# Optimization experiments

Measured on AMD Instinct MI355X. Metric: run time of the kernel, lower is better.

The kernel has to match this reference:

```python
import jax, jax.numpy as jnp
import numpy as np

PILLAR_WH = np.array([0.16, 0.16], np.float32)
MAX_POINTS = 100
MAX_PILLARS = 12000
MIN_XYZ = np.array([-51.2, -51.2, -5.0], np.float32)
MAX_XYZ = np.array([51.2, 51.2, 3.0], np.float32)
PAD_VALUE = 0.0
NGRID = np.ceil((MAX_XYZ[:2] - MIN_XYZ[:2]) / PILLAR_WH).astype(np.int32)  # [640, 640]
WH_N = (2.0 * PILLAR_WH / (MAX_XYZ[:2] - MIN_XYZ[:2])).astype(np.float32)  # pillar size in normalized coords
MIN_XY_N = (MIN_XYZ[:2] / MAX_XYZ[:2]).astype(np.float32)  # = [-1, -1]


def setup_inputs() -> dict:
    key = jax.random.key(0)
    B, P = 4, 50000
    k1, k2, k3 = jax.random.split(key, 3)
    # x,y restricted to [-8, 8] m so occupied pillars (<=100x100=10000) <= max_pillars,
    # making the torch module's random pillar subsampling a deterministic no-op.
    xy = jax.random.uniform(k1, (B, P, 2), minval=-8.0, maxval=8.0, dtype=jnp.float32)
    z = jax.random.uniform(k2, (B, P, 1), minval=-5.0, maxval=3.0, dtype=jnp.float32)
    r = jax.random.uniform(k3, (B, P, 1), dtype=jnp.float32)
    return {"point_clouds": jnp.concatenate([xy, z, r], axis=-1)}


def _per_sample(pc, pidx):
    # pc: (P, 4) normalized points; pidx: (P,) int32 pillar ids
    P = pc.shape[0]
    u, inv = jnp.unique(pidx, size=MAX_PILLARS, fill_value=-1, return_inverse=True)
    counts = jax.ops.segment_sum(jnp.ones((P,), jnp.int32), inv, num_segments=MAX_PILLARS)
    sums = jax.ops.segment_sum(pc[:, :3], inv, num_segments=MAX_PILLARS)
    mean = sums / jnp.maximum(counts, 1).astype(pc.dtype)[:, None]
    # stable sort points by pillar id; rank = position within pillar
    order = jnp.argsort(inv)
    seg = inv[order]
    pts = pc[order]
    start = jnp.cumsum(counts) - counts  # exclusive prefix of counts
    rank = jnp.arange(P, dtype=jnp.int32) - start[seg]
    in_cap = rank < MAX_POINTS
    flat = jnp.where(in_cap, seg * MAX_POINTS + rank, MAX_PILLARS * MAX_POINTS)  # OOB -> dropped
    buf = jnp.zeros((MAX_PILLARS * MAX_POINTS, 4), pc.dtype).at[flat].set(pts, mode='drop')
    occ = jnp.zeros((MAX_PILLARS * MAX_POINTS,), bool).at[flat].set(True, mode='drop')
    buf = buf.reshape(MAX_PILLARS, MAX_POINTS, 4)
    occ = occ.reshape(MAX_PILLARS, MAX_POINTS)
    ij = jnp.stack([u % NGRID[0], u // NGRID[0]], axis=-1).astype(pc.dtype)
    centers = jnp.asarray(MIN_XY_N) + ij * jnp.asarray(WH_N) + jnp.asarray(WH_N) * 0.5
    feat_c = jnp.abs(buf[..., :3] - mean[:, None, :])  # |xyz - pillar mean|
    feat_p = centers[:, None, :] - buf[..., :2]        # pillar center offset
    out = jnp.concatenate([buf, feat_c, feat_p], axis=-1)  # (max_pillars, max_points, 9)
    out = jnp.where(occ[..., None], out, jnp.asarray(PAD_VALUE, pc.dtype))
    return out, u


def reference(point_clouds):
    pc = point_clouds
    xyz_n = 2.0 * (pc[..., :3] - jnp.asarray(MIN_XYZ)) / jnp.asarray(MAX_XYZ - MIN_XYZ) - 1.0
    pc_n = jnp.concatenate([xyz_n, pc[..., 3:]], axis=-1)
    ij = jnp.minimum(
        jnp.floor((xyz_n[..., :2] - jnp.asarray(MIN_XY_N)) / jnp.asarray(WH_N)),
        jnp.asarray(NGRID, xyz_n.dtype) - 1.0,
    ).astype(jnp.int32)
    pidx = ij[..., 1] * int(NGRID[0]) + ij[..., 0]
    out, pillars = jax.vmap(_per_sample)(pc_n, pidx)
    return out, pillars
```

## Files before the change

kernel.cpp:

```cpp
#include <hip/hip_runtime.h>

#define NB 4
#define GRID_X 640
#define NCELL (GRID_X*GRID_X)
#define NWORD (NCELL/32)
#define MAXPIL 12000
#define MAXPTS 100
#define SCAN_BLK 256
#define NBLKA (NWORD/SCAN_BLK)

typedef unsigned short u16;
typedef unsigned int   u32;

__device__ __forceinline__ float bf16rt(float f) {
    u32 u = __builtin_bit_cast(u32, f);
    u32 r = ((u + 0x7FFFu + ((u >> 16) & 1u)) >> 16) << 16;
    return __builtin_bit_cast(float, r);
}

__device__ __forceinline__ float opaquef(float x) { asm volatile("" : "+v"(x)); return x; }

#define R102 0.009765625f
#define RWH  320.000030517578125f
__device__ __host__ constexpr float WH_N_C() { return (2.0f*0.16f)/(51.2f-(-51.2f)); }

__device__ __forceinline__ float norm_x(float v) {
    float p = 2.0f*(v + 51.2f) * R102;
    return opaquef(p) - 1.0f;
}
__device__ __forceinline__ float norm_z(float v) {
    float p = 2.0f*(v + 5.0f) * 0.125f;
    return opaquef(p) - 1.0f;
}

__device__ __forceinline__ int cell_of(float xn, float yn) {
    float fx = fminf(fmaxf(floorf((xn + 1.0f) * RWH), 0.0f), 639.0f);
    float fy = fminf(fmaxf(floorf((yn + 1.0f) * RWH), 0.0f), 639.0f);
    return (int)fy * GRID_X + (int)fx;
}

__global__ void k_init(int4* __restrict__ zero4, int nz4,
                       float* __restrict__ pillars_f, int* __restrict__ slotCell, int npil) {
    int i = blockIdx.x*blockDim.x + threadIdx.x;
    if (i < nz4) zero4[i] = make_int4(0,0,0,0);
    if (i < npil) { pillars_f[i] = -1.0f; slotCell[i] = -1; }
}

__global__ void k_mask(const float4* __restrict__ pc, int P, u32* __restrict__ occMask) {
    int i = blockIdx.x*blockDim.x + threadIdx.x;
    if (i >= NB*P) return;
    float4 pt = pc[i];
    int cell = cell_of(norm_x(pt.x), norm_x(pt.y));
    int b = i / P;
    atomicOr(&occMask[b*NWORD + (cell >> 5)], 1u << (cell & 31));
}

__global__ void k_scanA(const u32* __restrict__ occMask, int* __restrict__ scanBlk) {
    __shared__ int lds[SCAN_BLK];
    int blk = blockIdx.x % NBLKA;
    int b   = blockIdx.x / NBLKA;
    int w   = blk*SCAN_BLK + threadIdx.x;
    lds[threadIdx.x] = __popc(occMask[b*NWORD + w]);
    __syncthreads();
    for (int d = SCAN_BLK/2; d > 0; d >>= 1) {
        if (threadIdx.x < d) lds[threadIdx.x] += lds[threadIdx.x + d];
        __syncthreads();
    }
    if (threadIdx.x == 0) scanBlk[b*NBLKA + blk] = lds[0];
}

__global__ void k_scanB(int* __restrict__ scanBlk) {
    int b = blockIdx.x;
    if (threadIdx.x == 0) {
        int acc = 0;
        for (int i = 0; i < NBLKA; i++) {
            int v = scanBlk[b*NBLKA + i];
            scanBlk[b*NBLKA + i] = acc;
            acc += v;
        }
    }
}

__global__ void k_scanC(const u32* __restrict__ occMask, const int* __restrict__ scanBlk,
                        int* __restrict__ wordPrefix, float* __restrict__ pillars_f,
                        int* __restrict__ slotCell) {
    __shared__ int lds[SCAN_BLK];
    int blk = blockIdx.x % NBLKA;
    int b   = blockIdx.x / NBLKA;
    int tid = threadIdx.x;
    int w   = blk*SCAN_BLK + tid;
    u32 m = occMask[b*NWORD + w];
    int pop = __popc(m);
    lds[tid] = pop;
    __syncthreads();
    for (int d = 1; d < SCAN_BLK; d <<= 1) {
        int t = (tid >= d) ? lds[tid - d] : 0;
        __syncthreads();
        lds[tid] += t;
        __syncthreads();
    }
    int prefix = scanBlk[b*NBLKA + blk] + lds[tid] - pop;
    wordPrefix[b*NWORD + w] = prefix;
    int wbase = w << 5;
    int slot = prefix;
    while (m) {
        int bit = __ffs(m) - 1;
        m &= m - 1;
        if (slot < MAXPIL) {
            int cell = wbase + bit;
            slotCell[b*MAXPIL + slot] = cell;
            pillars_f[b*MAXPIL + slot] = bf16rt((float)cell);
        }
        slot++;
    }
}

__global__ void k_scatter(const float4* __restrict__ pc, int P,
                          const u32* __restrict__ occMask, const int* __restrict__ wordPrefix,
                          int* __restrict__ slotCnt, u16* __restrict__ idx16) {
    int i = blockIdx.x*blockDim.x + threadIdx.x;
    if (i >= NB*P) return;
    int b = i / P;
    int p = i - b*P;
    float4 pt = pc[i];
    int cell = cell_of(norm_x(pt.x), norm_x(pt.y));
    int w = cell >> 5, bit = cell & 31;
    u32 m = occMask[b*NWORD + w];
    int slot = wordPrefix[b*NWORD + w] + __popc(m & ((1u << bit) - 1u));
    if (slot >= MAXPIL) return;
    int g = b*MAXPIL + slot;
    int pos = atomicAdd(&slotCnt[g], 1);
    if (pos < MAXPTS) idx16[(size_t)g*MAXPTS + pos] = (u16)p;
}

__global__ __launch_bounds__(64) void k_write(const float4* __restrict__ pc, int P,
                        const int* __restrict__ slotCell, const int* __restrict__ slotCnt,
                        const u16* __restrict__ idx16, float* __restrict__ out) {
    __shared__ __align__(16) float tile[MAXPTS*9];
    __shared__ int sIdx[MAXPTS];
    __shared__ float sx[MAXPTS], sy[MAXPTS], sz[MAXPTS], sr[MAXPTS];
    int g = blockIdx.x;
    int b = g / MAXPIL;
    int lane = threadIdx.x;
    float4* out4 = (float4*)out + (size_t)g*225;
    int u = slotCell[g];
    if (u < 0) {
        float4 z = make_float4(0.f,0.f,0.f,0.f);
        for (int i = lane; i < 225; i += 64) out4[i] = z;
        return;
    }
    int ntot = slotCnt[g];
    int n = min(ntot, MAXPTS);

    float4* t4 = (float4*)tile;
    for (int i = lane; i < 225; i += 64) t4[i] = make_float4(0.f,0.f,0.f,0.f);

    float ax = 0.f, ay = 0.f, az = 0.f;
    for (int j = lane; j < n; j += 64) {
        int p = idx16[(size_t)g*MAXPTS + j];
        sIdx[j] = p;
        float4 pt = pc[b*P + p];
        float xn = norm_x(pt.x);
        float yn = norm_x(pt.y);
        float zn = norm_z(pt.z);
        sx[j] = xn; sy[j] = yn; sz[j] = zn; sr[j] = pt.w;
        ax += xn; ay += yn; az += zn;
    }
    for (int msk = 1; msk < 64; msk <<= 1) {
        ax += __shfl_xor(ax, msk);
        ay += __shfl_xor(ay, msk);
        az += __shfl_xor(az, msk);
    }
    float den = (float)max(ntot, 1);
    float mx = ax/den, my = ay/den, mz = az/den;
    const float wh = WH_N_C();
    float cx = -1.0f + (float)(u % GRID_X)*wh + wh*0.5f;
    float cy = -1.0f + (float)(u / GRID_X)*wh + wh*0.5f;
    __syncthreads();

    for (int j = lane; j < n; j += 64) {
        int p = sIdx[j];
        int rk = 0;
        for (int k = 0; k < n; k++) rk += (sIdx[k] < p) ? 1 : 0;
        float xn = sx[j], yn = sy[j], zn = sz[j];
        float* e = &tile[rk*9];
        e[0] = xn; e[1] = yn; e[2] = zn; e[3] = sr[j];
        e[4] = fabsf(xn - mx); e[5] = fabsf(yn - my); e[6] = fabsf(zn - mz);
        e[7] = cx - xn; e[8] = cy - yn;
    }
    __syncthreads();
    for (int i = lane; i < 225; i += 64) out4[i] = t4[i];
}

extern "C" void kernel_launch(void* const* d_in, const int* in_sizes, int n_in,
                              void* d_out, int out_size, void* d_ws, size_t ws_size,
                              hipStream_t stream) {
    const float4* pc = (const float4*)d_in[0];
    int P = in_sizes[0] / (NB*4);
    float* out = (float*)d_out;
    float* pillars_f = out + (size_t)NB*MAXPIL*MAXPTS*9;

    u32* occMask   = (u32*)d_ws;
    int* slotCnt   = (int*)(occMask + NB*NWORD);
    int* wordPrefix= slotCnt + NB*MAXPIL;
    int* scanBlk   = wordPrefix + NB*NWORD;
    int* slotCell  = scanBlk + 256;
    u16* idx16     = (u16*)(slotCell + NB*MAXPIL);

    int nzero = NB*NWORD + NB*MAXPIL;
    int nz4 = nzero / 4;
    int initThreads = nz4 > NB*MAXPIL ? nz4 : NB*MAXPIL;

    k_init<<<(initThreads+255)/256, 256, 0, stream>>>((int4*)occMask, nz4, pillars_f, slotCell, NB*MAXPIL);
    k_mask<<<(NB*P+255)/256, 256, 0, stream>>>(pc, P, occMask);
    k_scanA<<<NB*NBLKA, SCAN_BLK, 0, stream>>>(occMask, scanBlk);
    k_scanB<<<NB, 64, 0, stream>>>(scanBlk);
    k_scanC<<<NB*NBLKA, SCAN_BLK, 0, stream>>>(occMask, scanBlk, wordPrefix, pillars_f, slotCell);
    k_scatter<<<(NB*P+255)/256, 256, 0, stream>>>(pc, P, occMask, wordPrefix, slotCnt, idx16);
    k_write<<<NB*MAXPIL, 64, 0, stream>>>(pc, P, slotCell, slotCnt, idx16, out);
}
```

Baseline: 226.9 us.

## Merge three-pass scan into one block-per-sample kernel and cache point cell ids

Replaces the three scan kernels (block reduce, serial block prefix, block scan) with a single 512-thread kernel per sample. Each thread scans 25 mask words in registers, and the same kernel also zeroes slot counts and fills the unused pillar slots. k_mask now stores each point's cell id, so k_scatter reads it back instead of reloading the point and recomputing the cell. This removes two launches and the serial scanB pass, but runs the scan on only 4 blocks and adds 800 KB of cell-id writes and reads.

```diff
diff --git a/kernel.cpp b/kernel.cpp
--- a/kernel.cpp
+++ b/kernel.cpp
@@ -6,8 +6,8 @@
 #define NWORD (NCELL/32)
 #define MAXPIL 12000
 #define MAXPTS 100
-#define SCAN_BLK 256
-#define NBLKA (NWORD/SCAN_BLK)
+#define SCAN_T 512
+#define WPT (NWORD/SCAN_T)
 
 typedef unsigned short u16;
 typedef unsigned int   u32;
@@ -39,91 +39,78 @@
     return (int)fy * GRID_X + (int)fx;
 }
 
-__global__ void k_init(int4* __restrict__ zero4, int nz4,
-                       float* __restrict__ pillars_f, int* __restrict__ slotCell, int npil) {
+__global__ void k_init(int4* __restrict__ zero4, int nz4) {
     int i = blockIdx.x*blockDim.x + threadIdx.x;
     if (i < nz4) zero4[i] = make_int4(0,0,0,0);
-    if (i < npil) { pillars_f[i] = -1.0f; slotCell[i] = -1; }
-}
-
-__global__ void k_mask(const float4* __restrict__ pc, int P, u32* __restrict__ occMask) {
+}
+
+__global__ void k_mask(const float4* __restrict__ pc, int P, u32* __restrict__ occMask,
+                       int* __restrict__ cellId) {
     int i = blockIdx.x*blockDim.x + threadIdx.x;
     if (i >= NB*P) return;
     float4 pt = pc[i];
     int cell = cell_of(norm_x(pt.x), norm_x(pt.y));
+    cellId[i] = cell;
     int b = i / P;
     atomicOr(&occMask[b*NWORD + (cell >> 5)], 1u << (cell & 31));
 }
 
-__global__ void k_scanA(const u32* __restrict__ occMask, int* __restrict__ scanBlk) {
-    __shared__ int lds[SCAN_BLK];
-    int blk = blockIdx.x % NBLKA;
-    int b   = blockIdx.x / NBLKA;
-    int w   = blk*SCAN_BLK + threadIdx.x;
-    lds[threadIdx.x] = __popc(occMask[b*NWORD + w]);
+__global__ __launch_bounds__(SCAN_T) void k_scan(const u32* __restrict__ occMask,
+        int* __restrict__ wordPrefix, int* __restrict__ slotCnt,
+        int* __restrict__ slotCell, float* __restrict__ pillars_f) {
+    __shared__ int lds[SCAN_T];
+    int b = blockIdx.x;
+    int t = threadIdx.x;
+    const u32* mask = occMask + b*NWORD;
+    int base = t*WPT;
+    u32 w[WPT];
+#pragma unroll
+    for (int i = 0; i < WPT; i++) w[i] = mask[base + i];
+    for (int i = t; i < MAXPIL; i += SCAN_T) slotCnt[b*MAXPIL + i] = 0;
+    int sum = 0;
+#pragma unroll
+    for (int i = 0; i < WPT; i++) sum += __popc(w[i]);
+    lds[t] = sum;
     __syncthreads();
-    for (int d = SCAN_BLK/2; d > 0; d >>= 1) {
-        if (threadIdx.x < d) lds[threadIdx.x] += lds[threadIdx.x + d];
+    for (int d = 1; d < SCAN_T; d <<= 1) {
+        int v = (t >= d) ? lds[t - d] : 0;
         __syncthreads();
-    }
-    if (threadIdx.x == 0) scanBlk[b*NBLKA + blk] = lds[0];
-}
-
-__global__ void k_scanB(int* __restrict__ scanBlk) {
-    int b = blockIdx.x;
-    if (threadIdx.x == 0) {
-        int acc = 0;
-        for (int i = 0; i < NBLKA; i++) {
-            int v = scanBlk[b*NBLKA + i];
-            scanBlk[b*NBLKA + i] = acc;
-            acc += v;
+        lds[t] += v;
+        __syncthreads();
+    }
+    int slot  = lds[t] - sum;
+    int total = lds[SCAN_T - 1];
+#pragma unroll
+    for (int i = 0; i < WPT; i++) {
+        int wi = base + i;
+        wordPrefix[b*NWORD + wi] = slot;
+        u32 m = w[i];
+        int wbase = wi << 5;
+        while (m) {
+            int bit = __ffs(m) - 1;
+            m &= m - 1;
+            if (slot < MAXPIL) {
+                int cell = wbase + bit;
+                slotCell[b*MAXPIL + slot]  = cell;
+                pillars_f[b*MAXPIL + slot] = bf16rt((float)cell);
+            }
+            slot++;
         }
     }
-}
-
-__global__ void k_scanC(const u32* __restrict__ occMask, const int* __restrict__ scanBlk,
-                        int* __restrict__ wordPrefix, float* __restrict__ pillars_f,
-                        int* __restrict__ slotCell) {
-    __shared__ int lds[SCAN_BLK];
-    int blk = blockIdx.x % NBLKA;
-    int b   = blockIdx.x / NBLKA;
-    int tid = threadIdx.x;
-    int w   = blk*SCAN_BLK + tid;
-    u32 m = occMask[b*NWORD + w];
-    int pop = __popc(m);
-    lds[tid] = pop;
-    __syncthreads();
-    for (int d = 1; d < SCAN_BLK; d <<= 1) {
-        int t = (tid >= d) ? lds[tid - d] : 0;
-        __syncthreads();
-        lds[tid] += t;
-        __syncthreads();
-    }
-    int prefix = scanBlk[b*NBLKA + blk] + lds[tid] - pop;
-    wordPrefix[b*NWORD + w] = prefix;
-    int wbase = w << 5;
-    int slot = prefix;
-    while (m) {
-        int bit = __ffs(m) - 1;
-        m &= m - 1;
-        if (slot < MAXPIL) {
-            int cell = wbase + bit;
-            slotCell[b*MAXPIL + slot] = cell;
-            pillars_f[b*MAXPIL + slot] = bf16rt((float)cell);
-        }
-        slot++;
-    }
-}
-
-__global__ void k_scatter(const float4* __restrict__ pc, int P,
-                          const u32* __restrict__ occMask, const int* __restrict__ wordPrefix,
+    for (int i = total + t; i < MAXPIL; i += SCAN_T) {
+        slotCell[b*MAXPIL + i]  = -1;
+        pillars_f[b*MAXPIL + i] = -1.0f;
+    }
+}
+
+__global__ void k_scatter(int P, const u32* __restrict__ occMask,
+                          const int* __restrict__ wordPrefix, const int* __restrict__ cellId,
                           int* __restrict__ slotCnt, u16* __restrict__ idx16) {
     int i = blockIdx.x*blockDim.x + threadIdx.x;
     if (i >= NB*P) return;
     int b = i / P;
     int p = i - b*P;
-    float4 pt = pc[i];
-    int cell = cell_of(norm_x(pt.x), norm_x(pt.y));
+    int cell = cellId[i];
     int w = cell >> 5, bit = cell & 31;
     u32 m = occMask[b*NWORD + w];
     int slot = wordPrefix[b*NWORD + w] + __popc(m & ((1u << bit) - 1u));
@@ -203,19 +190,15 @@
     u32* occMask   = (u32*)d_ws;
     int* slotCnt   = (int*)(occMask + NB*NWORD);
     int* wordPrefix= slotCnt + NB*MAXPIL;
-    int* scanBlk   = wordPrefix + NB*NWORD;
-    int* slotCell  = scanBlk + 256;
-    u16* idx16     = (u16*)(slotCell + NB*MAXPIL);
-
-    int nzero = NB*NWORD + NB*MAXPIL;
-    int nz4 = nzero / 4;
-    int initThreads = nz4 > NB*MAXPIL ? nz4 : NB*MAXPIL;
-
-    k_init<<<(initThreads+255)/256, 256, 0, stream>>>((int4*)occMask, nz4, pillars_f, slotCell, NB*MAXPIL);
-    k_mask<<<(NB*P+255)/256, 256, 0, stream>>>(pc, P, occMask);
-    k_scanA<<<NB*NBLKA, SCAN_BLK, 0, stream>>>(occMask, scanBlk);
-    k_scanB<<<NB, 64, 0, stream>>>(scanBlk);
-    k_scanC<<<NB*NBLKA, SCAN_BLK, 0, stream>>>(occMask, scanBlk, wordPrefix, pillars_f, slotCell);
-    k_scatter<<<(NB*P+255)/256, 256, 0, stream>>>(pc, P, occMask, wordPrefix, slotCnt, idx16);
+    int* slotCell  = wordPrefix + NB*NWORD;
+    int* cellId    = slotCell + NB*MAXPIL;
+    u16* idx16     = (u16*)(cellId + NB*P);
+
+    int nz4 = (NB*NWORD) / 4;
+
+    k_init<<<(nz4+255)/256, 256, 0, stream>>>((int4*)occMask, nz4);
+    k_mask<<<(NB*P+255)/256, 256, 0, stream>>>(pc, P, occMask, cellId);
+    k_scan<<<NB, SCAN_T, 0, stream>>>(occMask, wordPrefix, slotCnt, slotCell, pillars_f);
+    k_scatter<<<(NB*P+255)/256, 256, 0, stream>>>(P, occMask, wordPrefix, cellId, slotCnt, idx16);
     k_write<<<NB*MAXPIL, 64, 0, stream>>>(pc, P, slotCell, slotCnt, idx16, out);
 }
```

New measurement: 270.6 us. +19.3%, slower.
